# Optimization experiments

Measured on AMD Instinct MI355X. Metric: run time of the kernel, lower is better.

Reference implementation:

```python
import jax, jax.numpy as jnp
import numpy as np

D = 1024      # d_model
E = 8         # num_experts
K = 2         # top_k
H = 4096      # expert_dim (bottleneck)
P = 256       # proj_dim
BATCH, SEQ = 2, 2048
CLAMP_MAX = float(np.log(1.0 / 0.01))
INIT_T = 0.5


def setup_inputs() -> dict:
    key = jax.random.key(0)
    ks = jax.random.split(key, 6)
    x = jax.random.normal(ks[0], (BATCH, SEQ, D), jnp.float32)
    # cosine projector (nn.Linear default init ~ U(-1/sqrt(D), 1/sqrt(D)))
    lim = 1.0 / np.sqrt(D)
    Wp = jax.random.uniform(ks[1], (P, D), jnp.float32, -lim, lim)
    bp = jnp.zeros((P,), jnp.float32)
    sim = 0.01 * jax.random.normal(ks[2], (P, E), jnp.float32)
    temp = jnp.full((1,), np.log(1.0 / INIT_T), jnp.float32)
    # RepAdapter 1x1 convs == linear layers; xavier_uniform, zero bias
    bA = float(np.sqrt(6.0 / (D + H)))
    A = jax.random.uniform(ks[3], (E, H, D), jnp.float32, -bA, bA)
    a_bias = jnp.zeros((E, H), jnp.float32)
    Bw = jax.random.uniform(ks[4], (E, D, H), jnp.float32, -bA, bA)
    b_bias = jnp.zeros((E, D), jnp.float32)
    return dict(x=x, Wp=Wp, bp=bp, sim=sim, temp=temp, A=A, a_bias=a_bias, Bw=Bw, b_bias=b_bias)


def reference(x, Wp, bp, sim, temp, A, a_bias, Bw, b_bias):
    B, S, d = x.shape
    e = sim.shape[1]
    xf = x.reshape(-1, d)                                  # [T, D]
    # cosine gate
    proj = xf @ Wp.T + bp                                  # [T, P]
    projn = proj / jnp.maximum(jnp.linalg.norm(proj, axis=1, keepdims=True), 1e-12)
    simn = sim / jnp.maximum(jnp.linalg.norm(sim, axis=0, keepdims=True), 1e-12)
    scale = jnp.exp(jnp.minimum(temp, CLAMP_MAX))          # [1]
    gate_probs = jax.nn.softmax((projn @ simn) * scale, axis=-1)   # [T, E]
    topv, topi = jax.lax.top_k(gate_probs, K)              # [T, K]
    topv = topv / (topv.sum(axis=-1, keepdims=True) + 1e-8)
    # per-token per-expert combine weight
    w = jnp.sum(topv[:, :, None] * jax.nn.one_hot(topi, e, dtype=x.dtype), axis=1)  # [T, E]

    # experts: y_e(x) = x + B_e(A_e x + a_e) + b_e (no nonlinearity); combine weighted
    def body(acc, params):
        Ae, ab, Be, bb, we = params
        h = xf @ Ae.T + ab                                 # [T, H]
        f = h @ Be.T + bb                                  # [T, D]
        return acc + we[:, None] * (xf + f), None

    out, _ = jax.lax.scan(body, jnp.zeros_like(xf), (A, a_bias, Bw, b_bias, w.T))
    out = out.reshape(B, S, d)

    frac = gate_probs.mean(axis=0)                         # expert_fractions
    aux_loss = jnp.sum((frac - 1.0 / e) ** 2)
    usage = jnp.bincount(topi.reshape(-1), length=e).astype(jnp.float32)
    return out, aux_loss, frac, usage
```

## Files before the change

kernel.cpp:

```cpp
#include <hip/hip_runtime.h>
#include <stdint.h>


typedef __attribute__((ext_vector_type(4))) float floatx4;
typedef __attribute__((ext_vector_type(8))) short shortx8;
typedef unsigned short ushort_t;

#define T_TOKENS 4096
#define D_DIM    1024
#define E_EXP    8
#define H_DIM    4096
#define P_DIM    256
#define ROWS_PAD 10240
#define MBLK     40

__device__ __forceinline__ ushort_t f2bf(float f) {
  union { float f; unsigned int u; } c; c.f = f;
  unsigned int u = c.u;
  unsigned int r = u + 0x7FFFu + ((u >> 16) & 1u);
  return (ushort_t)(r >> 16);
}

__device__ __forceinline__ void stage16(const ushort_t* g, ushort_t* l) {
  __builtin_amdgcn_global_load_lds((const __attribute__((address_space(1))) void*)g,
                                   (__attribute__((address_space(3))) void*)l, 16, 0, 0);
}

__global__ __launch_bounds__(256) void k_cvt(const float* __restrict__ src,
                                             ushort_t* __restrict__ dst, int n4) {
  int g = blockIdx.x * 256 + threadIdx.x;
  if (g >= n4) return;
  floatx4 v = ((const floatx4*)src)[g];
  ushort4 o; o.x = f2bf(v.x); o.y = f2bf(v.y); o.z = f2bf(v.z); o.w = f2bf(v.w);
  ((ushort4*)dst)[g] = o;
}

__global__ __launch_bounds__(256) void k_small_init(int* counts, int* cursor,
                                                    float* frac_sum, int* row2tok) {
  int g = blockIdx.x * 256 + threadIdx.x;
  if (g < 8) { counts[g] = 0; cursor[g] = 0; frac_sum[g] = 0.f; }
  if (g < ROWS_PAD) row2tok[g] = -1;
}

__global__ __launch_bounds__(256) void k_proj(const float* __restrict__ x,
                                              const float* __restrict__ Wp,
                                              const float* __restrict__ bp,
                                              float* __restrict__ proj) {
  __shared__ float Wc[256 * 36];
  __shared__ float Xc[16 * 36];
  int tid = threadIdx.x;
  int t0 = blockIdx.x * 16;
  int cg = tid & 31, tg = tid >> 5;
  floatx4 acc[2][8];
#pragma unroll
  for (int a = 0; a < 2; a++)
#pragma unroll
    for (int b = 0; b < 8; b++) acc[a][b] = (floatx4){0.f, 0.f, 0.f, 0.f};
  for (int kc = 0; kc < 32; ++kc) {
    int k0 = kc * 32;
    __syncthreads();
#pragma unroll
    for (int it = 0; it < 8; ++it) {
      int f = it * 256 + tid;
      int j = f >> 3, kk = (f & 7) << 2;
      floatx4 v = *(const floatx4*)(Wp + j * 1024 + k0 + kk);
      *(floatx4*)(Wc + j * 36 + kk) = v;
    }
    if (tid < 128) {
      int t = tid >> 3, kk = (tid & 7) << 2;
      floatx4 v = *(const floatx4*)(x + (size_t)(t0 + t) * 1024 + k0 + kk);
      *(floatx4*)(Xc + t * 36 + kk) = v;
    }
    __syncthreads();
#pragma unroll
    for (int k4 = 0; k4 < 8; ++k4) {
      floatx4 xv[2], wv[8];
#pragma unroll
      for (int tt = 0; tt < 2; tt++) xv[tt] = *(floatx4*)(Xc + (tg * 2 + tt) * 36 + k4 * 4);
#pragma unroll
      for (int jj = 0; jj < 8; jj++) wv[jj] = *(floatx4*)(Wc + (cg + jj * 32) * 36 + k4 * 4);
#pragma unroll
      for (int tt = 0; tt < 2; tt++)
#pragma unroll
        for (int jj = 0; jj < 8; jj++) acc[tt][jj] += xv[tt] * wv[jj];
    }
  }
#pragma unroll
  for (int tt = 0; tt < 2; tt++)
#pragma unroll
    for (int jj = 0; jj < 8; jj++) {
      floatx4 a = acc[tt][jj];
      float s = (a.x + a.y) + (a.z + a.w);
      int t = t0 + tg * 2 + tt, j = cg + jj * 32;
      proj[t * 256 + j] = s + bp[j];
    }
}

__global__ __launch_bounds__(128) void k_gate(const float* __restrict__ proj,
                                              const float* __restrict__ sim,
                                              const float* __restrict__ temp,
                                              int* __restrict__ topi, float* __restrict__ wslot,
                                              float* __restrict__ swsum,
                                              float* __restrict__ frac_sum, int* __restrict__ counts) {
  __shared__ float simT[8][256];
  __shared__ float snorm[8];
  __shared__ float fracs[8];
  __shared__ int cnts[8];
  int tid = threadIdx.x;
  for (int i = tid; i < 2048; i += 128) { int p = i >> 3, e = i & 7; simT[e][p] = sim[i]; }
  if (tid < 8) { fracs[tid] = 0.f; cnts[tid] = 0; }
  __syncthreads();
  if (tid < 8) {
    float s = 0.f;
    for (int p = 0; p < 256; p++) { float v = simT[tid][p]; s += v * v; }
    snorm[tid] = fmaxf(sqrtf(s), 1e-12f);
  }
  __syncthreads();
  int t = blockIdx.x * 128 + tid;
  floatx4 n4 = (floatx4){0.f, 0.f, 0.f, 0.f};
  floatx4 d4[8];
#pragma unroll
  for (int e = 0; e < 8; e++) d4[e] = (floatx4){0.f, 0.f, 0.f, 0.f};
  const floatx4* pr = (const floatx4*)(proj + t * 256);
  for (int k4 = 0; k4 < 64; ++k4) {
    floatx4 p = pr[k4];
    n4 += p * p;
#pragma unroll
    for (int e = 0; e < 8; e++) d4[e] += p * *(const floatx4*)(&simT[e][k4 * 4]);
  }
  float nrm = fmaxf(sqrtf((n4.x + n4.y) + (n4.z + n4.w)), 1e-12f);
  float scale = expf(fminf(temp[0], 4.6051701859880914f));
  float pe[8];
  float mx = -1e30f;
#pragma unroll
  for (int e = 0; e < 8; e++) {
    float d = (d4[e].x + d4[e].y) + (d4[e].z + d4[e].w);
    pe[e] = d / (nrm * snorm[e]) * scale;
    mx = fmaxf(mx, pe[e]);
  }
  float sum = 0.f;
#pragma unroll
  for (int e = 0; e < 8; e++) { pe[e] = expf(pe[e] - mx); sum += pe[e]; }
#pragma unroll
  for (int e = 0; e < 8; e++) pe[e] /= sum;
  int i0 = 0;
#pragma unroll
  for (int e = 1; e < 8; e++) if (pe[e] > pe[i0]) i0 = e;
  int i1 = (i0 == 0) ? 1 : 0;
#pragma unroll
  for (int e = 0; e < 8; e++) if (e != i1 && e != i0 && pe[e] > pe[i1]) i1 = e;
  float v0 = pe[i0], v1 = pe[i1];
  float s2 = v0 + v1 + 1e-8f;
  float w0 = v0 / s2, w1 = v1 / s2;
  topi[t * 2] = i0; topi[t * 2 + 1] = i1;
  wslot[t * 2] = w0; wslot[t * 2 + 1] = w1;
  swsum[t] = w0 + w1;
#pragma unroll
  for (int e = 0; e < 8; e++) atomicAdd(&fracs[e], pe[e]);
  atomicAdd(&cnts[i0], 1); atomicAdd(&cnts[i1], 1);
  __syncthreads();
  if (tid < 8) { atomicAdd(&frac_sum[tid], fracs[tid]); atomicAdd(&counts[tid], cnts[tid]); }
}

__global__ void k_scan(const int* __restrict__ counts, const float* __restrict__ frac_sum,
                       int* __restrict__ offsets, int* __restrict__ blk2e,
                       float* __restrict__ out_tail) {
  __shared__ int offs[9];
  if (threadIdx.x == 0) {
    int off = 0;
    for (int e = 0; e < 8; e++) { offs[e] = off; off += ((counts[e] + 255) >> 8) << 8; }
    offs[8] = off;
    for (int e = 0; e < 9; e++) offsets[e] = offs[e];
    float aux = 0.f;
    for (int e = 0; e < 8; e++) { float fr = frac_sum[e] / 4096.f; aux += (fr - 0.125f) * (fr - 0.125f); }
    out_tail[0] = aux;
  }
  __syncthreads();
  int tid = threadIdx.x;
  if (tid < MBLK) {
    int r = tid * 256, e = -1;
    for (int q = 0; q < 8; q++) if (r >= offs[q] && r < offs[q + 1]) e = q;
    blk2e[tid] = e;
  }
  if (tid < 8) {
    out_tail[1 + tid] = frac_sum[tid] / 4096.f;
    out_tail[9 + tid] = (float)counts[tid];
  }
}

__global__ __launch_bounds__(256) void k_assign(const int* __restrict__ topi,
                                                const float* __restrict__ wslot,
                                                const int* __restrict__ offsets,
                                                int* __restrict__ cursor,
                                                int* __restrict__ row2tok, float* __restrict__ roww) {
  int g = blockIdx.x * 256 + threadIdx.x;
  if (g >= 8192) return;
  int t = g >> 1;
  int e = topi[g];
  int pos = atomicAdd(&cursor[e], 1);
  int r = offsets[e] + pos;
  row2tok[r] = t;
  roww[r] = wslot[g];
}

__global__ __launch_bounds__(64) void k_gather(const float* __restrict__ x,
                                               const int* __restrict__ row2tok,
                                               ushort_t* __restrict__ xg) {
  int r = blockIdx.x;
  int t = row2tok[r];
  ushort4* dst = (ushort4*)(xg + (size_t)r * 1024);
  if (t < 0) {
    ushort4 z; z.x = z.y = z.z = z.w = 0;
    for (int i = threadIdx.x; i < 256; i += 64) dst[i] = z;
  } else {
    const floatx4* src = (const floatx4*)(x + (size_t)t * 1024);
    for (int i = threadIdx.x; i < 256; i += 64) {
      floatx4 v = src[i];
      ushort4 o; o.x = f2bf(v.x); o.y = f2bf(v.y); o.z = f2bf(v.z); o.w = f2bf(v.w);
      dst[i] = o;
    }
  }
}

__global__ __launch_bounds__(256) void k_init_out(const float* __restrict__ x,
                                                  const float* __restrict__ swsum,
                                                  float* __restrict__ out) {
  int g = blockIdx.x * 256 + threadIdx.x;
  float s = swsum[g >> 8];
  floatx4 v = ((const floatx4*)x)[g];
  ((floatx4*)out)[g] = v * s;
}

__global__ __launch_bounds__(512, 2) void k_gemm(const ushort_t* __restrict__ Aop0,
                                                 const ushort_t* __restrict__ Wall,
                                                 const float* __restrict__ bias,
                                                 const int* __restrict__ blk2e,
                                                 int K, int N,
                                                 ushort_t* __restrict__ hout,
                                                 float* __restrict__ outp,
                                                 const int* __restrict__ row2tok,
                                                 const float* __restrict__ roww) {
  int gx = gridDim.x;
  int nwg = gx * gridDim.y;
  int flat = blockIdx.y * gx + blockIdx.x;
  int qq = nwg >> 3, rr = nwg & 7;
  int xcd = flat & 7, idx = flat >> 3;
  int swz = (xcd < rr ? xcd * (qq + 1) : rr * (qq + 1) + (xcd - rr) * qq) + idx;
  int rb = swz / gx, nb = swz - rb * gx;

  int e = blk2e[rb];
  if (e < 0) return;
  int Kslice = K / gridDim.z;
  int kbase = blockIdx.z * Kslice;
  const ushort_t* Aop = Aop0 + (size_t)rb * 256 * K + kbase;
  const ushort_t* Bop = Wall + (size_t)e * N * K + (size_t)nb * 256 * K + kbase;

  __shared__ ushort_t As[2][256 * 64];
  __shared__ ushort_t Bs[2][256 * 64];

  int tid = threadIdx.x, lane = tid & 63, wv = tid >> 6;
  int l15 = lane & 15, q = lane >> 4;
  int wm = (wv >> 2) << 7;
  int wn = (wv & 3) << 6;

  floatx4 acc[8][4];
#pragma unroll
  for (int i = 0; i < 8; i++)
#pragma unroll
    for (int j = 0; j < 4; j++) acc[i][j] = (floatx4){0.f, 0.f, 0.f, 0.f};

  int srow = tid >> 3;
  int scol = ((tid & 7) ^ (srow & 7)) << 3;
  int ksteps = Kslice >> 6;
  int cur = 0;

  {
#pragma unroll
    for (int r = 0; r < 4; ++r) {
      int ldsoff = ((r << 9) + (wv << 6)) << 3;
      size_t goff = (size_t)((r << 6) + srow) * K + scol;
      stage16(Aop + goff, &As[0][ldsoff]);
      stage16(Bop + goff, &Bs[0][ldsoff]);
    }
  }
  __syncthreads();

  for (int ks = 0; ks < ksteps; ++ks) {
    if (ks + 1 < ksteps) {
      const ushort_t* An = Aop + (ks + 1) * 64;
      const ushort_t* Bn = Bop + (ks + 1) * 64;
      int nxt = cur ^ 1;
#pragma unroll
      for (int r = 0; r < 4; ++r) {
        int ldsoff = ((r << 9) + (wv << 6)) << 3;
        size_t goff = (size_t)((r << 6) + srow) * K + scol;
        stage16(An + goff, &As[nxt][ldsoff]);
        stage16(Bn + goff, &Bs[nxt][ldsoff]);
      }
    }
    const ushort_t* Ab = As[cur];
    const ushort_t* Bb = Bs[cur];
#pragma unroll
    for (int kc = 0; kc < 2; ++kc) {
      int cw = (kc << 2) + q;
      shortx8 af[8], bfv[4];
#pragma unroll
      for (int i = 0; i < 8; ++i) {
        int row = wm + i * 16 + l15;
        af[i] = *(const shortx8*)(Ab + (row << 6) + ((cw ^ (row & 7)) << 3));
      }
#pragma unroll
      for (int j = 0; j < 4; ++j) {
        int row = wn + j * 16 + l15;
        bfv[j] = *(const shortx8*)(Bb + (row << 6) + ((cw ^ (row & 7)) << 3));
      }
#pragma unroll
      for (int i = 0; i < 8; ++i)
#pragma unroll
        for (int j = 0; j < 4; ++j)
          acc[i][j] = __builtin_amdgcn_mfma_f32_16x16x32_bf16(af[i], bfv[j], acc[i][j], 0, 0, 0);
    }
    __syncthreads();
    cur ^= 1;
  }

  const float* be = bias + (size_t)e * N + (size_t)nb * 256;
  if (hout) {
    ushort_t* hp = hout + (size_t)(rb * 256) * N + nb * 256;
#pragma unroll
    for (int j = 0; j < 4; ++j) {
      int n = wn + j * 16 + l15;
      float bv = be[n];
#pragma unroll
      for (int i = 0; i < 8; ++i)
#pragma unroll
        for (int r = 0; r < 4; ++r) {
          int m = wm + i * 16 + (q << 2) + r;
          hp[(size_t)m * N + n] = f2bf(acc[i][j][r] + bv);
        }
    }
  } else {
    bool addb = (blockIdx.z == 0);
    float bvv[4];
#pragma unroll
    for (int j = 0; j < 4; ++j) bvv[j] = addb ? be[wn + j * 16 + l15] : 0.f;
#pragma unroll
    for (int i = 0; i < 8; ++i)
#pragma unroll
      for (int r = 0; r < 4; ++r) {
        int m = wm + i * 16 + (q << 2) + r;
        int grow = rb * 256 + m;
        int tok = row2tok[grow];
        if (tok < 0) continue;
        float w = roww[grow];
        float* op = outp + (size_t)tok * 1024 + nb * 256;
#pragma unroll
        for (int j = 0; j < 4; ++j) {
          int n = wn + j * 16 + l15;
          atomicAdd(op + n, (acc[i][j][r] + bvv[j]) * w);
        }
      }
  }
}

extern "C" void kernel_launch(void* const* d_in, const int* in_sizes, int n_in,
                              void* d_out, int out_size, void* d_ws, size_t ws_size,
                              hipStream_t stream) {
  (void)in_sizes; (void)n_in; (void)out_size; (void)ws_size;
  const float* x      = (const float*)d_in[0];
  const float* Wp     = (const float*)d_in[1];
  const float* bp     = (const float*)d_in[2];
  const float* sim    = (const float*)d_in[3];
  const float* temp   = (const float*)d_in[4];
  const float* A      = (const float*)d_in[5];
  const float* a_bias = (const float*)d_in[6];
  const float* Bw     = (const float*)d_in[7];
  const float* b_bias = (const float*)d_in[8];
  float* out = (float*)d_out;

  char* ws = (char*)d_ws;
  ushort_t* Abf    = (ushort_t*)(ws);
  ushort_t* Bbf    = (ushort_t*)(ws + 67108864);
  ushort_t* xg     = (ushort_t*)(ws + 134217728);
  ushort_t* h      = (ushort_t*)(ws + 155189248);
  float*    proj   = (float*)   (ws + 239075328);
  int*      topi   = (int*)     (ws + 243269632);
  float*    wslot  = (float*)   (ws + 243302400);
  float*    swsum  = (float*)   (ws + 243335168);
  int*      row2tok= (int*)     (ws + 243351552);
  float*    roww   = (float*)   (ws + 243392512);
  int*      counts = (int*)     (ws + 243433472);
  int*      cursor = (int*)     (ws + 243433504);
  int*      offsets= (int*)     (ws + 243433536);
  int*      blk2e  = (int*)     (ws + 243433600);
  float*    fracs  = (float*)   (ws + 243433760);

  k_cvt<<<32768, 256, 0, stream>>>(A,  Abf, 8388608);
  k_cvt<<<32768, 256, 0, stream>>>(Bw, Bbf, 8388608);
  k_small_init<<<40, 256, 0, stream>>>(counts, cursor, fracs, row2tok);
  k_proj<<<256, 256, 0, stream>>>(x, Wp, bp, proj);
  k_gate<<<32, 128, 0, stream>>>(proj, sim, temp, topi, wslot, swsum, fracs, counts);
  k_scan<<<1, 128, 0, stream>>>(counts, fracs, offsets, blk2e, out + 4194304);
  k_assign<<<32, 256, 0, stream>>>(topi, wslot, offsets, cursor, row2tok, roww);
  k_gather<<<ROWS_PAD, 64, 0, stream>>>(x, row2tok, xg);
  k_init_out<<<4096, 256, 0, stream>>>(x, swsum, out);
  k_gemm<<<dim3(16, MBLK, 1), 512, 0, stream>>>(xg, Abf, a_bias, blk2e, 1024, 4096,
                                                h, nullptr, nullptr, nullptr);
  k_gemm<<<dim3(4, MBLK, 2), 512, 0, stream>>>(h, Bbf, b_bias, blk2e, 4096, 1024,
                                               nullptr, out, row2tok, roww);
}
```

Baseline: 797.7 us.

## Interleave half-tile LDS staging with MFMA phases and raise split-K for down-projection

The expert GEMM main loop is restructured so that LDS tiles are stored as two 128-row halves. Loads of the next k-step are issued in four pieces, each placed between one of four MFMA phases. A partial vmcnt wait and a single barrier per step replace the full barrier after the prefetch, and s_setprio raises wave priority around the MFMA blocks. The aim is to hide global-to-LDS latency behind matrix math. Separately, the second GEMM's split-K grows from 2 to 4 to give more workgroups, which costs more atomic or partial output accumulation traffic.

```diff
diff --git a/kernel.cpp b/kernel.cpp
--- a/kernel.cpp
+++ b/kernel.cpp
@@ -255,13 +255,16 @@
   const ushort_t* Aop = Aop0 + (size_t)rb * 256 * K + kbase;
   const ushort_t* Bop = Wall + (size_t)e * N * K + (size_t)nb * 256 * K + kbase;
 
-  __shared__ ushort_t As[2][256 * 64];
-  __shared__ ushort_t Bs[2][256 * 64];
+  __shared__ ushort_t As[2][2][8192];
+  __shared__ ushort_t Bs[2][2][8192];
 
   int tid = threadIdx.x, lane = tid & 63, wv = tid >> 6;
   int l15 = lane & 15, q = lane >> 4;
   int wm = (wv >> 2) << 7;
   int wn = (wv & 3) << 6;
+  int ha = wv >> 2;
+  int hb = (wv >> 1) & 1;
+  int bn = wn & 127;
 
   floatx4 acc[8][4];
 #pragma unroll
@@ -270,57 +273,104 @@
     for (int j = 0; j < 4; j++) acc[i][j] = (floatx4){0.f, 0.f, 0.f, 0.f};
 
   int srow = tid >> 3;
-  int scol = ((tid & 7) ^ (srow & 7)) << 3;
+  int schunk = tid & 7;
   int ksteps = Kslice >> 6;
   int cur = 0;
 
-  {
-#pragma unroll
-    for (int r = 0; r < 4; ++r) {
-      int ldsoff = ((r << 9) + (wv << 6)) << 3;
-      size_t goff = (size_t)((r << 6) + srow) * K + scol;
-      stage16(Aop + goff, &As[0][ldsoff]);
-      stage16(Bop + goff, &Bs[0][ldsoff]);
-    }
-  }
-  __syncthreads();
-
-  for (int ks = 0; ks < ksteps; ++ks) {
-    if (ks + 1 < ksteps) {
-      const ushort_t* An = Aop + (ks + 1) * 64;
-      const ushort_t* Bn = Bop + (ks + 1) * 64;
-      int nxt = cur ^ 1;
-#pragma unroll
-      for (int r = 0; r < 4; ++r) {
-        int ldsoff = ((r << 9) + (wv << 6)) << 3;
-        size_t goff = (size_t)((r << 6) + srow) * K + scol;
-        stage16(An + goff, &As[nxt][ldsoff]);
-        stage16(Bn + goff, &Bs[nxt][ldsoff]);
-      }
-    }
-    const ushort_t* Ab = As[cur];
-    const ushort_t* Bb = Bs[cur];
-#pragma unroll
-    for (int kc = 0; kc < 2; ++kc) {
-      int cw = (kc << 2) + q;
-      shortx8 af[8], bfv[4];
-#pragma unroll
-      for (int i = 0; i < 8; ++i) {
-        int row = wm + i * 16 + l15;
-        af[i] = *(const shortx8*)(Ab + (row << 6) + ((cw ^ (row & 7)) << 3));
-      }
-#pragma unroll
-      for (int j = 0; j < 4; ++j) {
-        int row = wn + j * 16 + l15;
-        bfv[j] = *(const shortx8*)(Bb + (row << 6) + ((cw ^ (row & 7)) << 3));
-      }
-#pragma unroll
-      for (int i = 0; i < 8; ++i)
-#pragma unroll
-        for (int j = 0; j < 4; ++j)
-          acc[i][j] = __builtin_amdgcn_mfma_f32_16x16x32_bf16(af[i], bfv[j], acc[i][j], 0, 0, 0);
-    }
-    __syncthreads();
+  auto stage_half = [&](const ushort_t* gbase, int half, int kt, ushort_t* lds) {
+#pragma unroll
+    for (int r = 0; r < 2; ++r) {
+      int rowh = (r << 6) + srow;
+      size_t goff = (size_t)((half << 7) + rowh) * (size_t)K + (size_t)(kt << 6) +
+                    (size_t)((schunk ^ (rowh & 7)) << 3);
+      stage16(gbase + goff, lds + ((r << 9) + (wv << 6)) * 8);
+    }
+  };
+
+  stage_half(Aop, 0, 0, &As[0][0][0]);
+  stage_half(Aop, 1, 0, &As[0][1][0]);
+  stage_half(Bop, 0, 0, &Bs[0][0][0]);
+  stage_half(Bop, 1, 0, &Bs[0][1][0]);
+
+  for (int kt = 0; kt < ksteps; ++kt) {
+    int ktn = (kt + 1 < ksteps) ? kt + 1 : kt;
+    const ushort_t* Ab = &As[cur][ha][0];
+    const ushort_t* Bb = &Bs[cur][hb][0];
+    ushort_t* AsN = &As[cur ^ 1][0][0];
+    ushort_t* BsN = &Bs[cur ^ 1][0][0];
+
+    shortx8 af[4], bfv[4];
+
+    stage_half(Aop, 0, ktn, AsN);
+    asm volatile("s_waitcnt vmcnt(2)" ::: "memory");
+    __builtin_amdgcn_s_barrier();
+    __builtin_amdgcn_sched_barrier(0);
+#pragma unroll
+    for (int i = 0; i < 4; ++i) {
+      int row = i * 16 + l15;
+      af[i] = *(const shortx8*)(Ab + (row << 6) + ((q ^ (row & 7)) << 3));
+    }
+#pragma unroll
+    for (int j = 0; j < 4; ++j) {
+      int row = bn + j * 16 + l15;
+      bfv[j] = *(const shortx8*)(Bb + (row << 6) + ((q ^ (row & 7)) << 3));
+    }
+    __builtin_amdgcn_s_setprio(1);
+#pragma unroll
+    for (int i = 0; i < 4; ++i)
+#pragma unroll
+      for (int j = 0; j < 4; ++j)
+        acc[i][j] = __builtin_amdgcn_mfma_f32_16x16x32_bf16(af[i], bfv[j], acc[i][j], 0, 0, 0);
+    __builtin_amdgcn_s_setprio(0);
+
+    stage_half(Aop, 1, ktn, AsN + 8192);
+#pragma unroll
+    for (int i = 0; i < 4; ++i) {
+      int row = (i + 4) * 16 + l15;
+      af[i] = *(const shortx8*)(Ab + (row << 6) + ((q ^ (row & 7)) << 3));
+    }
+    __builtin_amdgcn_s_setprio(1);
+#pragma unroll
+    for (int i = 0; i < 4; ++i)
+#pragma unroll
+      for (int j = 0; j < 4; ++j)
+        acc[i + 4][j] = __builtin_amdgcn_mfma_f32_16x16x32_bf16(af[i], bfv[j], acc[i + 4][j], 0, 0, 0);
+    __builtin_amdgcn_s_setprio(0);
+
+    stage_half(Bop, 0, ktn, BsN);
+#pragma unroll
+    for (int i = 0; i < 4; ++i) {
+      int row = i * 16 + l15;
+      af[i] = *(const shortx8*)(Ab + (row << 6) + (((4 + q) ^ (row & 7)) << 3));
+    }
+#pragma unroll
+    for (int j = 0; j < 4; ++j) {
+      int row = bn + j * 16 + l15;
+      bfv[j] = *(const shortx8*)(Bb + (row << 6) + (((4 + q) ^ (row & 7)) << 3));
+    }
+    __builtin_amdgcn_s_setprio(1);
+#pragma unroll
+    for (int i = 0; i < 4; ++i)
+#pragma unroll
+      for (int j = 0; j < 4; ++j)
+        acc[i][j] = __builtin_amdgcn_mfma_f32_16x16x32_bf16(af[i], bfv[j], acc[i][j], 0, 0, 0);
+    __builtin_amdgcn_s_setprio(0);
+
+    stage_half(Bop, 1, ktn, BsN + 8192);
+#pragma unroll
+    for (int i = 0; i < 4; ++i) {
+      int row = (i + 4) * 16 + l15;
+      af[i] = *(const shortx8*)(Ab + (row << 6) + (((4 + q) ^ (row & 7)) << 3));
+    }
+    __builtin_amdgcn_s_setprio(1);
+#pragma unroll
+    for (int i = 0; i < 4; ++i)
+#pragma unroll
+      for (int j = 0; j < 4; ++j)
+        acc[i + 4][j] = __builtin_amdgcn_mfma_f32_16x16x32_bf16(af[i], bfv[j], acc[i + 4][j], 0, 0, 0);
+    __builtin_amdgcn_s_setprio(0);
+    __builtin_amdgcn_s_barrier();
+    __builtin_amdgcn_sched_barrier(0);
     cur ^= 1;
   }
 
@@ -406,6 +456,6 @@
   k_init_out<<<4096, 256, 0, stream>>>(x, swsum, out);
   k_gemm<<<dim3(16, MBLK, 1), 512, 0, stream>>>(xg, Abf, a_bias, blk2e, 1024, 4096,
                                                 h, nullptr, nullptr, nullptr);
-  k_gemm<<<dim3(4, MBLK, 2), 512, 0, stream>>>(h, Bbf, b_bias, blk2e, 4096, 1024,
+  k_gemm<<<dim3(4, MBLK, 4), 512, 0, stream>>>(h, Bbf, b_bias, blk2e, 4096, 1024,
                                                nullptr, out, row2tok, roww);
 }
```

After: 833.4 us. 1.04x slower.
